# Kernel optimization log

Hardware: AMD Instinct MI355X
Metric: run time of the kernel (lower is better)

The kernel has to match this reference:

```python
import jax, jax.numpy as jnp
import numpy as np

N = 384          # residues / nodes
E = 12288        # edges (avg degree 32)
D_LM = 1024      # BERT hidden
D_NODE = 256     # extra node features -> D_LM + D_NODE = 1280
D = 1280         # node_emb_size
H = D // 10      # 128, dis/mask MLP hidden
M = 64           # masked positions


def setup_inputs() -> dict:
    key = jax.random.key(0)
    ks = jax.random.split(key, 16)
    s = lambda d_in: 1.0 / np.sqrt(d_in)
    inp = {
        "lm_embedding": jax.random.normal(ks[0], (1, N + 2, D_LM), jnp.float32),
        "node_feat": jax.random.normal(ks[1], (N, D_NODE), jnp.float32),
        # positive distances in [0.5, 1.5) so edge_weight = 1/(d^2+1e-6) is well scaled
        "edge_feat": jax.random.uniform(ks[2], (E, 1), jnp.float32) + 0.5,
        "src": jax.random.randint(ks[3], (E,), 0, N, jnp.int32),
        "dst": jax.random.randint(ks[4], (E,), 0, N, jnp.int32),
        "mask_index": jax.random.randint(ks[5], (M,), 0, N, jnp.int32),
        # GINConv apply-func linears (stored as [in, out]; torch Linear is x @ W.T + b)
        "W_gin0": jax.random.normal(ks[6], (D, D), jnp.float32) * s(D),
        "b_gin0": jnp.zeros((D,), jnp.float32),
        "W_gin1": jax.random.normal(ks[7], (D, D), jnp.float32) * s(D),
        "b_gin1": jnp.zeros((D,), jnp.float32),
        # dis_nn: Linear(D,H) -> ReLU -> Linear(H,30)
        "Wd1": jax.random.normal(ks[8], (D, H), jnp.float32) * s(D),
        "bd1": jnp.zeros((H,), jnp.float32),
        "Wd2": jax.random.normal(ks[9], (H, 30), jnp.float32) * s(H),
        "bd2": jnp.zeros((30,), jnp.float32),
        # mask_nn: Linear(D,H) -> ReLU -> Linear(H,2) -> Tanh
        "Wm1": jax.random.normal(ks[10], (D, H), jnp.float32) * s(D),
        "bm1": jnp.zeros((H,), jnp.float32),
        "Wm2": jax.random.normal(ks[11], (H, 2), jnp.float32) * s(H),
        "bm2": jnp.zeros((2,), jnp.float32),
    }
    return inp


def _gin(x, src, dst, edge_weight, W, b):
    # DGL GINConv (eps=0, 'sum'): Linear( x + sum_{e:(u->v)} w_e * x_u )
    msg = x[src] * edge_weight                      # [E, D] gather-multiply
    agg = jax.ops.segment_sum(msg, dst, num_segments=N)  # scatter-sum to dst
    return (x + agg) @ W + b


def reference(lm_embedding, node_feat, edge_feat, src, dst, mask_index,
              W_gin0, b_gin0, W_gin1, b_gin1,
              Wd1, bd1, Wd2, bd2, Wm1, bm1, Wm2, bm2):
    # node_feat0: strip CLS/SEP tokens, concat with node features -> [N, D]
    node_feat0 = jnp.concatenate([lm_embedding[0, 1:-1, :], node_feat], axis=1)
    edge_weight = 1.0 / (edge_feat ** 2 + 1e-6)     # [E, 1]

    # original uses node_feat0.data (detached) as GIN input
    x0 = jax.lax.stop_gradient(node_feat0)
    h = _gin(x0, src, dst, edge_weight, W_gin0, b_gin0)
    node_output = _gin(h, src, dst, edge_weight, W_gin1, b_gin1)
    node_output = node_output + node_feat0          # residual (use_lm=1)

    # pairwise squared differences: [N, N, D]
    dis_hid = (node_output[None, :, :] - node_output[:, None, :]) ** 2
    dh = dis_hid.reshape(-1, D)                     # [N*N, D]
    dis_pred = jax.nn.relu(dh @ Wd1 + bd1) @ Wd2 + bd2  # [N*N, 30]

    xm = node_output[mask_index]                    # [M, D]
    mask_pred = jnp.tanh(jax.nn.relu(xm @ Wm1 + bm1) @ Wm2 + bm2)  # [M, 2]
    return dis_pred, mask_pred
```

## Files before the change

kernel.cpp:

```cpp
#include <hip/hip_runtime.h>
#include <hip/hip_bf16.h>

#define NN 384
#define EE 12288
#define DD 1280
#define HH 128
#define DISROWS (NN*NN)

typedef short bf16x8 __attribute__((ext_vector_type(8)));
typedef short bf16x4 __attribute__((ext_vector_type(4)));
typedef float f32x4  __attribute__((ext_vector_type(4)));

__device__ __forceinline__ unsigned short f2bf(float x){
  unsigned u = __builtin_bit_cast(unsigned, x);
  u += 0x7fffu + ((u >> 16) & 1u);
  return (unsigned short)(u >> 16);
}
__device__ __forceinline__ float bf2f(unsigned short h){
  unsigned u = ((unsigned)h) << 16;
  return __builtin_bit_cast(float, u);
}
__device__ __forceinline__ short f2bf_fast(float x){
  return (short)__bfloat16_as_ushort(__float2bfloat16(x));
}
__device__ __forceinline__ void glds16(const short* g, short* l){
  __builtin_amdgcn_global_load_lds((const __attribute__((address_space(1))) void*)g,
                                   (__attribute__((address_space(3))) void*)l, 16, 0, 0);
}

__device__ __forceinline__ void tsplit_body(const float* __restrict__ W,
                                            short* __restrict__ Thi, short* __restrict__ Tlo,
                                            int R, int C, int bx, int by, int t,
                                            float* tile ){
  int rb = by*64, cb = bx*64;
  int r  = t >> 2;
  int cs = (t & 3) * 16;
  const float* sp = W + (long)(rb + r)*C + cb + cs;
  #pragma unroll
  for (int i = 0; i < 16; i += 4){
    f32x4 v = *(const f32x4*)(sp + i);
    tile[r*65 + cs+i+0] = v[0]; tile[r*65 + cs+i+1] = v[1];
    tile[r*65 + cs+i+2] = v[2]; tile[r*65 + cs+i+3] = v[3];
  }
  __syncthreads();
  int cp = t >> 2;
  int rs = (t & 3) * 16;
  bf16x8 vh0, vh1, vl0, vl1;
  #pragma unroll
  for (int i = 0; i < 8; ++i){
    float f = tile[(rs+i)*65 + cp];
    unsigned short h = f2bf(f);
    vh0[i] = (short)h; vl0[i] = (short)f2bf(f - bf2f(h));
  }
  #pragma unroll
  for (int i = 0; i < 8; ++i){
    float f = tile[(rs+8+i)*65 + cp];
    unsigned short h = f2bf(f);
    vh1[i] = (short)h; vl1[i] = (short)f2bf(f - bf2f(h));
  }
  long ob = (long)(cb + cp)*R + rb + rs;
  *(bf16x8*)&Thi[ob]   = vh0;
  *(bf16x8*)&Thi[ob+8] = vh1;
  if (Tlo){
    *(bf16x8*)&Tlo[ob]   = vl0;
    *(bf16x8*)&Tlo[ob+8] = vl1;
  }
}

__global__ void k_prep(const int* __restrict__ dst, const float* __restrict__ ef,
                       int* __restrict__ offs, int* __restrict__ sorted,
                       float* __restrict__ ew,
                       const float* __restrict__ Wd1, short* __restrict__ W1t,
                       const float* __restrict__ Wd2, short* __restrict__ W2t,
                       const float* __restrict__ Wg0, short* __restrict__ WtAh,
                       short* __restrict__ WtAl,
                       const float* __restrict__ Wg1, short* __restrict__ WtBh,
                       short* __restrict__ WtBl){
  __shared__ __align__(16) float sh[64*65];
  const int b = blockIdx.x;
  const int t = threadIdx.x;
  if (b == 0){
    int* cnt = (int*)sh;
    int* base = cnt + 512;
    if (t < 512) cnt[t] = 0;
    __syncthreads();
    for (int e = t; e < EE; e += 512){
      atomicAdd(&cnt[dst[e]], 1);
      float f = ef[e];
      ew[e] = 1.0f/(f*f + 1e-6f);
    }
    __syncthreads();
    for (int off = 1; off < 512; off <<= 1){
      int v = (t >= off) ? cnt[t - off] : 0;
      __syncthreads();
      cnt[t] += v;
      __syncthreads();
    }
    if (t < NN){
      int excl = t ? cnt[t-1] : 0;
      offs[t] = excl;
      base[t] = excl;
    }
    if (t == 0) offs[NN] = EE;
    __syncthreads();
    for (int e = t; e < EE; e += 512){
      int p = atomicAdd(&base[dst[e]], 1);
      sorted[p] = e;
    }
    return;
  }
  if (b < 42){
    int g = b - 1;
    if (g < 40){
      if (t < 256) tsplit_body(Wd1, W1t, nullptr, DD, HH, g & 1, g >> 1, t, sh);
      else { __syncthreads(); }
      return;
    }
    for (int i = t; i < 32*HH; i += 512){
      int c = i >> 7, h = i & 127;
      float v = (c < 30) ? Wd2[h*30 + c] : 0.f;
      W2t[i] = (short)f2bf(v);
    }
    return;
  }
  if (b < 442){
    int g = b - 42;
    if (t < 256) tsplit_body(Wg0, WtAh, WtAl, DD, DD, g % 20, g / 20, t, sh);
    else { __syncthreads(); }
    return;
  }
  {
    int g = b - 442;
    if (t < 256) tsplit_body(Wg1, WtBh, WtBl, DD, DD, g % 20, g / 20, t, sh);
    else { __syncthreads(); }
  }
}

__global__ void k_agg(const float* __restrict__ X,
                      const float* __restrict__ lm, const float* __restrict__ nf,
                      const float* __restrict__ ew, const int* __restrict__ src,
                      const int* __restrict__ offs, const int* __restrict__ sorted,
                      short* __restrict__ Yh, short* __restrict__ Yl){
  __shared__ int   s_nd[160];
  __shared__ float s_w[160];
  const int v = blockIdx.x;
  const int y = blockIdx.y;
  const int t = threadIdx.x;
  const int d = y*256 + t;
  float acc;
  if (X)           acc = X[(long)v*DD + d];
  else if (y < 4)  acc = lm[(long)(v+1)*1024 + d];
  else             acc = nf[(long)v*256 + t];
  const int b = offs[v], e = offs[v+1];
  for (int c0 = b; c0 < e; c0 += 160){
    int n = e - c0; if (n > 160) n = 160;
    __syncthreads();
    if (t < n){
      int eid = sorted[c0 + t];
      s_nd[t] = src[eid];
      s_w[t]  = ew[eid];
    }
    __syncthreads();
    if (X){
      int k = 0;
      for (; k + 4 <= n; k += 4){
        acc += s_w[k]  *X[(long)s_nd[k]*DD + d];
        acc += s_w[k+1]*X[(long)s_nd[k+1]*DD + d];
        acc += s_w[k+2]*X[(long)s_nd[k+2]*DD + d];
        acc += s_w[k+3]*X[(long)s_nd[k+3]*DD + d];
      }
      for (; k < n; ++k) acc += s_w[k]*X[(long)s_nd[k]*DD + d];
    } else if (y < 4){
      int k = 0;
      for (; k + 4 <= n; k += 4){
        acc += s_w[k]  *lm[(long)(s_nd[k]+1)*1024 + d];
        acc += s_w[k+1]*lm[(long)(s_nd[k+1]+1)*1024 + d];
        acc += s_w[k+2]*lm[(long)(s_nd[k+2]+1)*1024 + d];
        acc += s_w[k+3]*lm[(long)(s_nd[k+3]+1)*1024 + d];
      }
      for (; k < n; ++k) acc += s_w[k]*lm[(long)(s_nd[k]+1)*1024 + d];
    } else {
      int k = 0;
      for (; k + 4 <= n; k += 4){
        acc += s_w[k]  *nf[(long)s_nd[k]*256 + t];
        acc += s_w[k+1]*nf[(long)s_nd[k+1]*256 + t];
        acc += s_w[k+2]*nf[(long)s_nd[k+2]*256 + t];
        acc += s_w[k+3]*nf[(long)s_nd[k+3]*256 + t];
      }
      for (; k < n; ++k) acc += s_w[k]*nf[(long)s_nd[k]*256 + t];
    }
  }
  unsigned short h = f2bf(acc);
  Yh[(long)v*DD + d] = (short)h;
  Yl[(long)v*DD + d] = (short)f2bf(acc - bf2f(h));
}

__launch_bounds__(256, 4)
__global__ void k_gin_gemm(const short* __restrict__ Yh, const short* __restrict__ Yl,
                           const short* __restrict__ Whi, const short* __restrict__ Wlo,
                           float* __restrict__ P){
  __shared__ __align__(16) short Ahi[64*40], Alo[64*40], Bhi[128*40], Blo[128*40];
  const int m0 = blockIdx.x*64;
  const int n0 = blockIdx.y*128;
  const int kbase = blockIdx.z*160;
  const int t = threadIdx.x, w = t >> 6, lane = t & 63;
  const int l15 = lane & 15, l4 = lane >> 4;
  f32x4 acc[8];
  #pragma unroll
  for (int n = 0; n < 8; ++n) acc[n] = (f32x4){0.f,0.f,0.f,0.f};

  const int arow = t >> 2, aq = t & 3;
  const short* aph = Yh  + (long)(m0+arow)*DD + aq*8;
  const short* apl = Yl  + (long)(m0+arow)*DD + aq*8;
  const int brow = t >> 1, bh2 = t & 1;
  const short* bph = Whi + (long)(n0+brow)*DD + bh2*16;
  const short* bpl = Wlo + (long)(n0+brow)*DD + bh2*16;

  for (int kk = 0; kk < 5; ++kk){
    int d0 = kbase + kk*32;
    __syncthreads();
    *(bf16x8*)&Ahi[arow*40 + aq*8] = *(const bf16x8*)(aph + d0);
    *(bf16x8*)&Alo[arow*40 + aq*8] = *(const bf16x8*)(apl + d0);
    *(bf16x8*)&Bhi[brow*40 + bh2*16]     = *(const bf16x8*)(bph + d0);
    *(bf16x8*)&Bhi[brow*40 + bh2*16 + 8] = *(const bf16x8*)(bph + d0 + 8);
    *(bf16x8*)&Blo[brow*40 + bh2*16]     = *(const bf16x8*)(bpl + d0);
    *(bf16x8*)&Blo[brow*40 + bh2*16 + 8] = *(const bf16x8*)(bpl + d0 + 8);
    __syncthreads();

    bf16x8 ah = *(const bf16x8*)&Ahi[(w*16 + l15)*40 + l4*8];
    bf16x8 al = *(const bf16x8*)&Alo[(w*16 + l15)*40 + l4*8];
    #pragma unroll
    for (int n = 0; n < 8; ++n){
      bf16x8 bh = *(const bf16x8*)&Bhi[(n*16 + l15)*40 + l4*8];
      bf16x8 bl = *(const bf16x8*)&Blo[(n*16 + l15)*40 + l4*8];
      acc[n] = __builtin_amdgcn_mfma_f32_16x16x32_bf16(ah, bh, acc[n], 0,0,0);
      acc[n] = __builtin_amdgcn_mfma_f32_16x16x32_bf16(ah, bl, acc[n], 0,0,0);
      acc[n] = __builtin_amdgcn_mfma_f32_16x16x32_bf16(al, bh, acc[n], 0,0,0);
    }
  }
  float* Pz = P + (long)blockIdx.z*NN*DD;
  #pragma unroll
  for (int n = 0; n < 8; ++n){
    int gc = n0 + n*16 + l15;
    #pragma unroll
    for (int r = 0; r < 4; ++r)
      Pz[(long)(m0 + w*16 + l4*4 + r)*DD + gc] = acc[n][r];
  }
}

__global__ void k_red(const float* __restrict__ P, const float* __restrict__ bias,
                      const float* __restrict__ lm, const float* __restrict__ nf,
                      float* __restrict__ Out){
  const int i = blockIdx.x*256 + threadIdx.x;
  const int col = (i*4) % DD;
  const int row = (i*4) / DD;
  const f32x4* P4 = (const f32x4*)P;
  f32x4 s = P4[i];
  #pragma unroll
  for (int z = 1; z < 8; ++z) s += P4[i + z*122880];
  s += *(const f32x4*)(bias + col);
  if (lm){
    f32x4 r = (col < 1024) ? *(const f32x4*)(lm + (long)(row+1)*1024 + col)
                           : *(const f32x4*)(nf + (long)row*256 + col - 1024);
    s += r;
  }
  ((f32x4*)Out)[i] = s;
}

__launch_bounds__(256, 3)
__global__ void k_dis(const float* __restrict__ X, const short* __restrict__ W1t,
                      const float* __restrict__ bd1, const short* __restrict__ W2t,
                      const float* __restrict__ bd2, float* __restrict__ out,
                      const int* __restrict__ midx,
                      const float* __restrict__ Wm1, const float* __restrict__ bm1,
                      const float* __restrict__ Wm2, const float* __restrict__ bm2){
  __shared__ __align__(16) short smem[25088];
  const int b = blockIdx.x;
  const int t = threadIdx.x;

  if (b >= 600){
    float* tl = (float*)smem;
    int m = b - 600;
    if (t < HH){
      const float* x = X + (long)midx[m]*DD;
      float a0 = 0.f, a1 = 0.f, a2 = 0.f, a3 = 0.f;
      for (int d = 0; d < DD; d += 4){
        a0 += x[d]   * Wm1[(d)*HH + t];
        a1 += x[d+1] * Wm1[(d+1)*HH + t];
        a2 += x[d+2] * Wm1[(d+2)*HH + t];
        a3 += x[d+3] * Wm1[(d+3)*HH + t];
      }
      float v = a0 + a1 + a2 + a3 + bm1[t];
      tl[t] = v > 0.f ? v : 0.f;
    }
    __syncthreads();
    if (t < 2){
      float s = bm2[t];
      for (int h = 0; h < HH; ++h) s += tl[h]*Wm2[h*2 + t];
      out[(long)DISROWS*30 + m*2 + t] = tanhf(s);
    }
    return;
  }

  int k = 0, rem = b;
  while (rem >= 2*(24 - k)){ rem -= 2*(24 - k); ++k; }
  int ib = 2*k;
  if (rem >= 24 - k){ ++ib; rem -= 24 - k; }
  const int jb = k + rem;
  const int i0 = ib*8, j0 = jb*16;

  const int w = t >> 6, lane = t & 63;
  const int l15 = lane & 15, l4 = lane >> 4;

  short* WA = smem;
  float* XF = (float*)(smem + 16384);
  short* TL = smem;
  float* OT = (float*)(smem + 17408);

  f32x4 acc[2][8];
  #pragma unroll
  for (int m = 0; m < 2; ++m)
    #pragma unroll
    for (int n = 0; n < 8; ++n) acc[m][n] = (f32x4){0.f,0.f,0.f,0.f};

  const short* wsrc[4];
  #pragma unroll
  for (int i = 0; i < 4; ++i){
    int hb = w*32 + i*8 + (lane >> 3);
    wsrc[i] = W1t + (long)hb*DD + (((lane & 7) ^ (hb & 7))*8);
  }
  const float* xsrc[6];
  int xli[6];
  #pragma unroll
  for (int g = 0; g < 6; ++g){
    int idx = g*256 + t;
    int rowl = idx >> 6, col = idx & 63;
    int grow = (rowl < 8) ? (i0 + rowl) : (j0 + rowl - 8);
    xsrc[g] = X + (long)grow*DD + col;
    xli[g] = rowl*68 + col;
  }

  float xr[6];
  #pragma unroll
  for (int i = 0; i < 4; ++i)
    glds16(wsrc[i], WA + (w*32 + i*8)*64);
  #pragma unroll
  for (int g = 0; g < 6; ++g) xr[g] = xsrc[g][0];
  #pragma unroll
  for (int g = 0; g < 6; ++g) XF[xli[g]] = xr[g];
  __syncthreads();

  for (int mk = 0; mk < 20; ++mk){
    const int cb = mk & 1;
    short* WAc = WA + cb*8192;
    float* XFc = XF + cb*1632;
    short* WAn = WA + (cb^1)*8192;
    float* XFn = XF + (cb^1)*1632;
    if (mk < 19){
      #pragma unroll
      for (int i = 0; i < 4; ++i)
        glds16(wsrc[i] + (mk+1)*64, WAn + (w*32 + i*8)*64);
      #pragma unroll
      for (int g = 0; g < 6; ++g) xr[g] = xsrc[g][(mk+1)*64];
    }
    #pragma unroll
    for (int ks = 0; ks < 2; ++ks){
      f32x4 xj0 = *(const f32x4*)&XFc[(8 + l15)*68 + ks*32 + l4*8];
      f32x4 xj1 = *(const f32x4*)&XFc[(8 + l15)*68 + ks*32 + l4*8 + 4];
      bf16x8 a[2];
      #pragma unroll
      for (int m = 0; m < 2; ++m){
        const float* xip = &XFc[(2*w + m)*68 + ks*32 + l4*8];
        f32x4 xi0 = *(const f32x4*)xip;
        f32x4 xi1 = *(const f32x4*)(xip + 4);
        f32x4 d0 = xj0 - xi0; d0 = d0*d0;
        f32x4 d1 = xj1 - xi1; d1 = d1*d1;
        bf16x8 av;
        #pragma unroll
        for (int q = 0; q < 4; ++q){
          av[q]   = f2bf_fast(d0[q]);
          av[4+q] = f2bf_fast(d1[q]);
        }
        a[m] = av;
      }
      #pragma unroll
      for (int n = 0; n < 8; ++n){
        bf16x8 wf = *(const bf16x8*)&WAc[(n*16 + l15)*64 + (((ks*4 + l4) ^ (l15 & 7))*8)];
        acc[0][n] = __builtin_amdgcn_mfma_f32_16x16x32_bf16(wf, a[0], acc[0][n], 0,0,0);
        acc[1][n] = __builtin_amdgcn_mfma_f32_16x16x32_bf16(wf, a[1], acc[1][n], 0,0,0);
      }
    }
    if (mk < 19){
      #pragma unroll
      for (int g = 0; g < 6; ++g) XFn[xli[g]] = xr[g];
    }
    __syncthreads();
  }

  f32x4 bd1v[8];
  #pragma unroll
  for (int n = 0; n < 8; ++n) bd1v[n] = *(const f32x4*)(bd1 + n*16 + l4*4);
  #pragma unroll
  for (int m = 0; m < 2; ++m){
    int pair = (2*w + m)*16 + l15;
    #pragma unroll
    for (int n = 0; n < 8; ++n){
      bf16x4 pv;
      #pragma unroll
      for (int r = 0; r < 4; ++r){
        float v = acc[m][n][r] + bd1v[n][r];
        v = v > 0.f ? v : 0.f;
        pv[r] = f2bf_fast(v);
      }
      *(bf16x4*)&TL[pair*136 + n*16 + l4*4] = pv;
    }
  }
  __syncthreads();

  f32x4 acc2[2][2];
  #pragma unroll
  for (int m2 = 0; m2 < 2; ++m2)
    #pragma unroll
    for (int nn = 0; nn < 2; ++nn) acc2[m2][nn] = (f32x4){0.f,0.f,0.f,0.f};
  #pragma unroll
  for (int hs = 0; hs < 4; ++hs){
    bf16x8 b2[2];
    #pragma unroll
    for (int nn = 0; nn < 2; ++nn)
      b2[nn] = *(const bf16x8*)&W2t[(nn*16 + l15)*HH + hs*32 + l4*8];
    #pragma unroll
    for (int m2 = 0; m2 < 2; ++m2){
      bf16x8 a2 = *(const bf16x8*)&TL[(w*32 + m2*16 + l15)*136 + hs*32 + l4*8];
      #pragma unroll
      for (int nn = 0; nn < 2; ++nn)
        acc2[m2][nn] = __builtin_amdgcn_mfma_f32_16x16x32_bf16(a2, b2[nn], acc2[m2][nn], 0,0,0);
    }
  }
  #pragma unroll
  for (int m2 = 0; m2 < 2; ++m2){
    #pragma unroll
    for (int nn = 0; nn < 2; ++nn){
      int cc = nn*16 + l15;
      if (cc < 30){
        float b2v = bd2[cc];
        #pragma unroll
        for (int r = 0; r < 4; ++r)
          OT[(w*32 + m2*16 + l4*4 + r)*30 + cc] = acc2[m2][nn][r] + b2v;
      }
    }
  }
  __syncthreads();

  {
    int i = t >> 5;
    int ca = (t & 31)*15;
    long nbase = ((long)(i0 + i)*NN + j0)*30 + ca;
    const float* nsrc = OT + i*480 + ca;
    #pragma unroll
    for (int q = 0; q < 15; ++q) out[nbase + q] = nsrc[q];
    int j = t >> 4;
    int s = t & 15;
    int ii = s >> 1;
    int c0 = (s & 1)*15;
    long mbase = ((long)(j0 + j)*NN + i0 + ii)*30 + c0;
    const float* msrc = OT + ii*480 + j*30 + c0;
    #pragma unroll
    for (int q = 0; q < 15; ++q) out[mbase + q] = msrc[q];
  }
}

extern "C" void kernel_launch(void* const* d_in, const int* in_sizes, int n_in,
                              void* d_out, int out_size, void* d_ws, size_t ws_size,
                              hipStream_t stream){
  const float* lm   = (const float*)d_in[0];
  const float* nf   = (const float*)d_in[1];
  const float* ef   = (const float*)d_in[2];
  const int*   src  = (const int*)d_in[3];
  const int*   dst  = (const int*)d_in[4];
  const int*   midx = (const int*)d_in[5];
  const float* Wg0  = (const float*)d_in[6];
  const float* bg0  = (const float*)d_in[7];
  const float* Wg1  = (const float*)d_in[8];
  const float* bg1  = (const float*)d_in[9];
  const float* Wd1  = (const float*)d_in[10];
  const float* bd1  = (const float*)d_in[11];
  const float* Wd2  = (const float*)d_in[12];
  const float* bd2  = (const float*)d_in[13];
  const float* Wm1  = (const float*)d_in[14];
  const float* bm1  = (const float*)d_in[15];
  const float* Wm2  = (const float*)d_in[16];
  const float* bm2  = (const float*)d_in[17];
  float* dis = (float*)d_out;

  char* ws = (char*)d_ws;
  size_t off = 0;
  auto alloc = [&](size_t bytes)->void*{
    void* p = ws + off; off += (bytes + 255) & ~(size_t)255; return p;
  };
  float* hb0  = (float*)alloc((size_t)NN*DD*4);
  float* hb   = (float*)alloc((size_t)NN*DD*4);
  short* Yh   = (short*)alloc((size_t)NN*DD*2);
  short* Yl   = (short*)alloc((size_t)NN*DD*2);
  float* ew   = (float*)alloc((size_t)EE*4);
  int*   offs = (int*)alloc((NN+1)*4);
  int*   sorted = (int*)alloc(EE*4);
  short* WtAh = (short*)alloc((size_t)DD*DD*2);
  short* WtAl = (short*)alloc((size_t)DD*DD*2);
  short* WtBh = (short*)alloc((size_t)DD*DD*2);
  short* WtBl = (short*)alloc((size_t)DD*DD*2);
  short* W1t  = (short*)alloc((size_t)HH*DD*2);
  short* W2t  = (short*)alloc((size_t)32*HH*2);
  float* P    = (float*)alloc((size_t)8*NN*DD*4);

  k_prep<<<842,512,0,stream>>>(dst, ef, offs, sorted, ew,
                               Wd1, W1t, Wd2, W2t,
                               Wg0, WtAh, WtAl, Wg1, WtBh, WtBl);

  k_agg<<<dim3(384,5),256,0,stream>>>(nullptr, lm, nf, ew, src, offs, sorted, Yh, Yl);
  k_gin_gemm<<<dim3(6,10,8),256,0,stream>>>(Yh, Yl, WtAh, WtAl, P);
  k_red<<<480,256,0,stream>>>(P, bg0, nullptr, nullptr, hb0);

  k_agg<<<dim3(384,5),256,0,stream>>>(hb0, lm, nf, ew, src, offs, sorted, Yh, Yl);
  k_gin_gemm<<<dim3(6,10,8),256,0,stream>>>(Yh, Yl, WtBh, WtBl, P);
  k_red<<<480,256,0,stream>>>(P, bg1, lm, nf, hb);

  k_dis<<<664,256,0,stream>>>(hb, W1t, bd1, W2t, bd2, dis,
                              midx, Wm1, bm1, Wm2, bm2);
}
```

Baseline: 123.2 us.

## Fuse split-K reduction into GIN GEMM via last-block atomic counter; widen weight split

The separate k_red kernels that summed the 8 split-K partials are removed. Each GEMM tile now bumps an atomic counter, and the last of its 8 K-slices sums the partials, adds bias and residual, and writes the output. The Wg0/Wg1 transpose-split in k_prep now uses all 512 threads instead of leaving half of them idle. This saves two kernel launches and one extra pass over P, in exchange for threadfence and atomic overhead and a memset of the counters.

Result: slower. 181.2 us (+47.0%).

```diff
diff --git a/kernel.cpp b/kernel.cpp
--- a/kernel.cpp
+++ b/kernel.cpp
@@ -31,7 +31,7 @@
 __device__ __forceinline__ void tsplit_body(const float* __restrict__ W,
                                             short* __restrict__ Thi, short* __restrict__ Tlo,
                                             int R, int C, int bx, int by, int t,
-                                            float* tile ){
+                                            float* tile){
   int rb = by*64, cb = bx*64;
   int r  = t >> 2;
   int cs = (t & 3) * 16;
@@ -65,6 +65,32 @@
     *(bf16x8*)&Tlo[ob]   = vl0;
     *(bf16x8*)&Tlo[ob+8] = vl1;
   }
+}
+
+__device__ __forceinline__ void tsplit512(const float* __restrict__ W,
+                                          short* __restrict__ Thi, short* __restrict__ Tlo,
+                                          int R, int C, int bx, int by, int t, float* tile){
+  int rb = by*64, cb = bx*64;
+  int r = t >> 3, cs = (t & 7)*8;
+  const float* sp = W + (long)(rb + r)*C + cb + cs;
+  f32x4 v0 = *(const f32x4*)sp;
+  f32x4 v1 = *(const f32x4*)(sp + 4);
+  tile[r*65 + cs+0] = v0[0]; tile[r*65 + cs+1] = v0[1];
+  tile[r*65 + cs+2] = v0[2]; tile[r*65 + cs+3] = v0[3];
+  tile[r*65 + cs+4] = v1[0]; tile[r*65 + cs+5] = v1[1];
+  tile[r*65 + cs+6] = v1[2]; tile[r*65 + cs+7] = v1[3];
+  __syncthreads();
+  int cp = t >> 3, rs = (t & 7)*8;
+  bf16x8 vh, vl;
+  #pragma unroll
+  for (int i = 0; i < 8; ++i){
+    float f = tile[(rs+i)*65 + cp];
+    unsigned short h = f2bf(f);
+    vh[i] = (short)h; vl[i] = (short)f2bf(f - bf2f(h));
+  }
+  long ob = (long)(cb + cp)*R + rb + rs;
+  *(bf16x8*)&Thi[ob] = vh;
+  if (Tlo) *(bf16x8*)&Tlo[ob] = vl;
 }
 
 __global__ void k_prep(const int* __restrict__ dst, const float* __restrict__ ef,
@@ -125,14 +151,12 @@
   }
   if (b < 442){
     int g = b - 42;
-    if (t < 256) tsplit_body(Wg0, WtAh, WtAl, DD, DD, g % 20, g / 20, t, sh);
-    else { __syncthreads(); }
+    tsplit512(Wg0, WtAh, WtAl, DD, DD, g % 20, g / 20, t, sh);
     return;
   }
   {
     int g = b - 442;
-    if (t < 256) tsplit_body(Wg1, WtBh, WtBl, DD, DD, g % 20, g / 20, t, sh);
-    else { __syncthreads(); }
+    tsplit512(Wg1, WtBh, WtBl, DD, DD, g % 20, g / 20, t, sh);
   }
 }
 
@@ -198,8 +222,12 @@
 __launch_bounds__(256, 4)
 __global__ void k_gin_gemm(const short* __restrict__ Yh, const short* __restrict__ Yl,
                            const short* __restrict__ Whi, const short* __restrict__ Wlo,
-                           float* __restrict__ P){
+                           float* __restrict__ P, int* __restrict__ cnt,
+                           const float* __restrict__ bias,
+                           const float* __restrict__ lm, const float* __restrict__ nf,
+                           float* __restrict__ Out){
   __shared__ __align__(16) short Ahi[64*40], Alo[64*40], Bhi[128*40], Blo[128*40];
+  __shared__ int islast;
   const int m0 = blockIdx.x*64;
   const int n0 = blockIdx.y*128;
   const int kbase = blockIdx.z*160;
@@ -246,25 +274,34 @@
     for (int r = 0; r < 4; ++r)
       Pz[(long)(m0 + w*16 + l4*4 + r)*DD + gc] = acc[n][r];
   }
-}
-
-__global__ void k_red(const float* __restrict__ P, const float* __restrict__ bias,
-                      const float* __restrict__ lm, const float* __restrict__ nf,
-                      float* __restrict__ Out){
-  const int i = blockIdx.x*256 + threadIdx.x;
-  const int col = (i*4) % DD;
-  const int row = (i*4) / DD;
-  const f32x4* P4 = (const f32x4*)P;
-  f32x4 s = P4[i];
-  #pragma unroll
-  for (int z = 1; z < 8; ++z) s += P4[i + z*122880];
-  s += *(const f32x4*)(bias + col);
-  if (lm){
-    f32x4 r = (col < 1024) ? *(const f32x4*)(lm + (long)(row+1)*1024 + col)
-                           : *(const f32x4*)(nf + (long)row*256 + col - 1024);
-    s += r;
-  }
-  ((f32x4*)Out)[i] = s;
+
+  __syncthreads();
+  if (t == 0){
+    __threadfence();
+    int v = atomicAdd(&cnt[blockIdx.x*10 + blockIdx.y], 1);
+    islast = (v == 7);
+  }
+  __syncthreads();
+  if (!islast) return;
+  __threadfence();
+  #pragma unroll
+  for (int q = 0; q < 8; ++q){
+    int idx = q*256 + t;
+    int row = idx >> 5, c4 = idx & 31;
+    int grow = m0 + row, gcol = n0 + c4*4;
+    long off = (long)grow*DD + gcol;
+    f32x4 s = *(const f32x4*)&P[off];
+    #pragma unroll
+    for (int z = 1; z < 8; ++z)
+      s += *(const f32x4*)&P[(long)z*NN*DD + off];
+    s += *(const f32x4*)(bias + gcol);
+    if (lm){
+      f32x4 r = (gcol < 1024) ? *(const f32x4*)(lm + (long)(grow+1)*1024 + gcol)
+                              : *(const f32x4*)(nf + (long)grow*256 + gcol - 1024);
+      s += r;
+    }
+    *(f32x4*)&Out[off] = s;
+  }
 }
 
 __launch_bounds__(256, 3)
@@ -497,6 +534,8 @@
   auto alloc = [&](size_t bytes)->void*{
     void* p = ws + off; off += (bytes + 255) & ~(size_t)255; return p;
   };
+  int*   cnt0 = (int*)alloc(256);
+  int*   cnt1 = (int*)alloc(256);
   float* hb0  = (float*)alloc((size_t)NN*DD*4);
   float* hb   = (float*)alloc((size_t)NN*DD*4);
   short* Yh   = (short*)alloc((size_t)NN*DD*2);
@@ -512,17 +551,19 @@
   short* W2t  = (short*)alloc((size_t)32*HH*2);
   float* P    = (float*)alloc((size_t)8*NN*DD*4);
 
+  hipMemsetAsync(cnt0, 0, 512, stream);
+
   k_prep<<<842,512,0,stream>>>(dst, ef, offs, sorted, ew,
                                Wd1, W1t, Wd2, W2t,
                                Wg0, WtAh, WtAl, Wg1, WtBh, WtBl);
 
   k_agg<<<dim3(384,5),256,0,stream>>>(nullptr, lm, nf, ew, src, offs, sorted, Yh, Yl);
-  k_gin_gemm<<<dim3(6,10,8),256,0,stream>>>(Yh, Yl, WtAh, WtAl, P);
-  k_red<<<480,256,0,stream>>>(P, bg0, nullptr, nullptr, hb0);
+  k_gin_gemm<<<dim3(6,10,8),256,0,stream>>>(Yh, Yl, WtAh, WtAl, P, cnt0,
+                                            bg0, nullptr, nullptr, hb0);
 
   k_agg<<<dim3(384,5),256,0,stream>>>(hb0, lm, nf, ew, src, offs, sorted, Yh, Yl);
-  k_gin_gemm<<<dim3(6,10,8),256,0,stream>>>(Yh, Yl, WtBh, WtBl, P);
-  k_red<<<480,256,0,stream>>>(P, bg1, lm, nf, hb);
+  k_gin_gemm<<<dim3(6,10,8),256,0,stream>>>(Yh, Yl, WtBh, WtBl, P, cnt1,
+                                            bg1, lm, nf, hb);
 
   k_dis<<<664,256,0,stream>>>(hb, W1t, bd1, W2t, bd2, dis,
                               midx, Wm1, bm1, Wm2, bm2);
```
